# Performance work log

Measured on AMD Instinct MI355X. Metric: run time of the kernel, lower is better.

Reference implementation:

```python
import jax, jax.numpy as jnp
import numpy as np

B, T, C = 2, 2048, 1024
H, M = 16, 64
D = C // H  # head_dim = 64


def setup_inputs() -> dict:
    key = jax.random.key(0)
    ks = jax.random.split(key, 6)
    x = jax.random.normal(ks[0], (B, T, C), dtype=jnp.float32)
    Wqkv = jax.random.normal(ks[1], (3 * C, C), dtype=jnp.float32) / np.sqrt(C)
    bqkv = jax.random.normal(ks[2], (3 * C,), dtype=jnp.float32) * 0.02
    Wout = jax.random.normal(ks[3], (C, C), dtype=jnp.float32) / np.sqrt(C)
    bout = jax.random.normal(ks[4], (C,), dtype=jnp.float32) * 0.02
    proj = jax.random.normal(ks[5], (H, D, M), dtype=jnp.float32) / np.sqrt(D)
    return {"x": x, "Wqkv": Wqkv, "bqkv": bqkv, "Wout": Wout, "bout": bout, "proj": proj}


def reference(x, Wqkv, bqkv, Wout, bout, proj):
    b, t, c = x.shape
    h, d, m = proj.shape
    qkv = x @ Wqkv.T + bqkv                          # [B,T,3C]
    q, k, v = jnp.split(qkv, 3, axis=-1)
    # [B,T,C] -> [B,H,T,D]
    to_heads = lambda z: z.reshape(b, t, h, d).transpose(0, 2, 1, 3)
    q, k, v = to_heads(q), to_heads(k), to_heads(v)
    qf, kf, vf = q.astype(jnp.float32), k.astype(jnp.float32), v.astype(jnp.float32)
    pf = proj.astype(jnp.float32)
    q_prime = jax.nn.relu(jnp.einsum('bhtd,hdm->bhtm', qf, pf))
    k_prime = jax.nn.relu(jnp.einsum('bhtd,hdm->bhtm', kf, pf))
    k_cumsum = jnp.cumsum(k_prime, axis=2)                        # [B,H,T,M]
    kv_prod = jnp.einsum('bhtm,bhtd->bhtmd', k_prime, vf)          # [B,H,T,M,D]
    kv_cumsum = jnp.cumsum(kv_prod, axis=2)                        # [B,H,T,M,D]
    context = jnp.einsum('bhtm,bhtmd->bhtd', q_prime, kv_cumsum)   # [B,H,T,D]
    norm = jnp.einsum('bhtm,bhtm->bht', q_prime, k_cumsum)         # [B,H,T]
    out = context / (norm[..., None] + 1e-6)
    out = out.astype(x.dtype).transpose(0, 2, 1, 3).reshape(b, t, c)
    return out @ Wout.T + bout
```

## Files before the change

### kernel.cpp

```cpp
#include <hip/hip_runtime.h>
#include <cstddef>

#define B_  2
#define T_  2048
#define C_  1024
#define H_  16
#define D_  64
#define M_  64
#define NC_ 32
#define CH_ 64

typedef __attribute__((ext_vector_type(8))) short bf16x8;
typedef __attribute__((ext_vector_type(4))) float f32x4;

__device__ __forceinline__ ushort f2bf(float f) {
    union { float f; unsigned u; } v; v.f = f;
    unsigned r = v.u + 0x7FFF + ((v.u >> 16) & 1);
    return (ushort)(r >> 16);
}
__device__ __forceinline__ float bf2f(ushort u) {
    union { unsigned u; float f; } x; x.u = ((unsigned)u) << 16; return x.f;
}

__device__ __forceinline__ void gld_lds16(const ushort* g, ushort* lds) {
    __builtin_amdgcn_global_load_lds(
        (const __attribute__((address_space(1))) unsigned int*)g,
        (__attribute__((address_space(3))) unsigned int*)lds,
        16, 0, 0);
}

__device__ __forceinline__ bf16x8 frag_ld(const ushort* lds, int row16, int k0, int lane) {
    int r = row16 + (lane & 15);
    int byte = ((k0 * 2) + ((lane >> 4) << 4)) ^ ((r & 7) << 4);
    return *(const bf16x8*)((const char*)lds + r * 128 + byte);
}

#define VMCNT(n) asm volatile("s_waitcnt vmcnt(" #n ")" ::: "memory")
#define BAR() do { __builtin_amdgcn_s_barrier(); __builtin_amdgcn_sched_barrier(0); } while (0)

#define SEG1_ 256
#define SEG2_ 512
#define SEG3_ 1536
#define SEG4_ 1792
#define NPREP_ 1804

__global__ __launch_bounds__(256) void prep_all(
    const float* __restrict__ x, const float* __restrict__ Wqkv,
    const float* __restrict__ bqkv, const float* __restrict__ Wout,
    const float* __restrict__ proj,
    ushort* __restrict__ Wbt, ushort* __restrict__ xbf,
    ushort* __restrict__ WoutBf, float* __restrict__ bbig)
{
    __shared__ float Ws[64 * 128];
    __shared__ float Ps[64 * 64];
    const int blk = blockIdx.x, t = threadIdx.x;
    if (blk < SEG1_) {
        const int sel = blk >> 7, h = (blk >> 3) & 15, cc = blk & 7;
        const int rowbase = sel * 1024 + h * 64;
        {
            const int r0 = t >> 5, cq = t & 31;
#pragma unroll
            for (int k = 0; k < 8; ++k) {
                int r = r0 + 8 * k;
                *(float4*)&Ws[r * 128 + cq * 4] =
                    *(const float4*)&Wqkv[(size_t)(rowbase + r) * 1024 + cc * 128 + cq * 4];
            }
        }
#pragma unroll
        for (int k = 0; k < 4; ++k) {
            int i4 = t + 256 * k;
            *(float4*)&Ps[i4 * 4] = *(const float4*)&proj[h * 4096 + i4 * 4];
        }
        __syncthreads();
#pragma unroll
        for (int k = 0; k < 2; ++k) {
            int id = t + 256 * k;
            int m4 = id >> 5, c4 = id & 31;
            float4 a0 = {0.f,0.f,0.f,0.f}, a1 = a0, a2 = a0, a3 = a0;
            for (int d = 0; d < 64; ++d) {
                float4 w = *(const float4*)&Ws[d * 128 + c4 * 4];
                float4 p = *(const float4*)&Ps[d * 64 + m4 * 4];
                a0.x += p.x*w.x; a0.y += p.x*w.y; a0.z += p.x*w.z; a0.w += p.x*w.w;
                a1.x += p.y*w.x; a1.y += p.y*w.y; a1.z += p.y*w.z; a1.w += p.y*w.w;
                a2.x += p.z*w.x; a2.y += p.z*w.y; a2.z += p.z*w.z; a2.w += p.z*w.w;
                a3.x += p.w*w.x; a3.y += p.w*w.y; a3.z += p.w*w.z; a3.w += p.w*w.w;
            }
            size_t obase = (size_t)(rowbase + m4 * 4) * 1024 + cc * 128 + c4 * 4;
            ushort4 o0 = { f2bf(a0.x), f2bf(a0.y), f2bf(a0.z), f2bf(a0.w) };
            ushort4 o1 = { f2bf(a1.x), f2bf(a1.y), f2bf(a1.z), f2bf(a1.w) };
            ushort4 o2 = { f2bf(a2.x), f2bf(a2.y), f2bf(a2.z), f2bf(a2.w) };
            ushort4 o3 = { f2bf(a3.x), f2bf(a3.y), f2bf(a3.z), f2bf(a3.w) };
            *(ushort4*)&Wbt[obase]          = o0;
            *(ushort4*)&Wbt[obase + 1024]   = o1;
            *(ushort4*)&Wbt[obase + 2048]   = o2;
            *(ushort4*)&Wbt[obase + 3072]   = o3;
        }
    } else if (blk < SEG2_) {
        int bo = blk - SEG1_;
#pragma unroll
        for (int pass = 0; pass < 4; ++pass) {
            int i4 = bo * 1024 + pass * 256 + t;
            float4 v = ((const float4*)Wqkv)[524288 + i4];
            ushort4 o = { f2bf(v.x), f2bf(v.y), f2bf(v.z), f2bf(v.w) };
            ((ushort4*)(Wbt + 2097152))[i4] = o;
        }
    } else if (blk < SEG3_) {
        int bo = blk - SEG2_;
#pragma unroll
        for (int pass = 0; pass < 4; ++pass) {
            int i4 = bo * 1024 + pass * 256 + t;
            float4 v = ((const float4*)x)[i4];
            ushort4 o = { f2bf(v.x), f2bf(v.y), f2bf(v.z), f2bf(v.w) };
            ((ushort4*)xbf)[i4] = o;
        }
    } else if (blk < SEG4_) {
        int bo = blk - SEG3_;
#pragma unroll
        for (int pass = 0; pass < 4; ++pass) {
            int i4 = bo * 1024 + pass * 256 + t;
            float4 v = ((const float4*)Wout)[i4];
            ushort4 o = { f2bf(v.x), f2bf(v.y), f2bf(v.z), f2bf(v.w) };
            ((ushort4*)WoutBf)[i4] = o;
        }
    } else {
        int j = (blk - SEG4_) * 256 + t;
        if (j < 2048) {
            int sel = j >> 10, hm = j & 1023, h = hm >> 6, m = hm & 63;
            const float* b = bqkv + sel * C_ + h * D_;
            const float* p = proj + (size_t)h * D_ * M_ + m;
            float acc = 0.f;
#pragma unroll 8
            for (int d = 0; d < D_; ++d) acc += b[d] * p[(size_t)d * M_];
            bbig[j] = acc;
        } else {
            bbig[j] = bqkv[j];
        }
    }
}

__device__ __forceinline__ void stage_G0(const ushort* __restrict__ Ag, const ushort* __restrict__ Bg,
                                         ushort* Abuf, ushort* Bbuf,
                                         int m0, int n0, int K, int kcol, int w, int lane) {
    const int l8 = lane >> 3, lc = (lane & 7) * 8;
#pragma unroll
    for (int i = 0; i < 4; ++i) {
        int c = w * 4 + i;
        if (c < 8) {
            int fr = (c < 4) ? c * 8 : 64 + (c - 4) * 8;
            int r = fr + l8;
            int cs = lc ^ ((r & 7) << 3);
            gld_lds16(Ag + (size_t)(m0 + r) * K + kcol + cs, Abuf + fr * 64);
        } else {
            int cb = c - 8, g = cb / 6, k8 = cb - g * 6;
            int fr = g * 96 + k8 * 8;
            int r = fr + l8;
            int cs = lc ^ ((r & 7) << 3);
            gld_lds16(Bg + (size_t)(n0 + r) * K + kcol + cs, Bbuf + fr * 64);
        }
    }
}

__device__ __forceinline__ void stage_G1(const ushort* __restrict__ Ag, const ushort* __restrict__ Bg,
                                         ushort* Abuf, ushort* Bbuf,
                                         int m0, int n0, int K, int kcol, int w, int lane) {
    const int l8 = lane >> 3, lc = (lane & 7) * 8;
#pragma unroll
    for (int i = 0; i < 3; ++i) {
        int cb = w * 3 + i, g = cb / 6, k8 = cb - g * 6;
        int fr = g * 96 + 48 + k8 * 8;
        int r = fr + l8;
        int cs = lc ^ ((r & 7) << 3);
        gld_lds16(Bg + (size_t)(n0 + r) * K + kcol + cs, Bbuf + fr * 64);
    }
    {
        int fr = (w < 4) ? 32 + w * 8 : 96 + (w - 4) * 8;
        int r = fr + l8;
        int cs = lc ^ ((r & 7) << 3);
        gld_lds16(Ag + (size_t)(m0 + r) * K + kcol + cs, Abuf + fr * 64);
    }
}

__device__ __forceinline__ void phase_mfma(const ushort* Abuf, const ushort* Bbuf,
                                           f32x4 (&acc)[4][6], int wr, int wc, int lane,
                                           int Mh, int Nh) {
    bf16x8 a[2][2], b[3][2];
#pragma unroll
    for (int i = 0; i < 2; ++i)
#pragma unroll
        for (int ks = 0; ks < 2; ++ks)
            a[i][ks] = frag_ld(Abuf, wr + Mh * 32 + i * 16, ks * 32, lane);
#pragma unroll
    for (int j = 0; j < 3; ++j)
#pragma unroll
        for (int ks = 0; ks < 2; ++ks)
            b[j][ks] = frag_ld(Bbuf, wc + Nh * 48 + j * 16, ks * 32, lane);
    __builtin_amdgcn_s_setprio(1);
#pragma unroll
    for (int ks = 0; ks < 2; ++ks)
#pragma unroll
        for (int i = 0; i < 2; ++i)
#pragma unroll
            for (int j = 0; j < 3; ++j)
                acc[Mh * 2 + i][Nh * 3 + j] = __builtin_amdgcn_mfma_f32_16x16x32_bf16(
                    a[i][ks], b[j][ks], acc[Mh * 2 + i][Nh * 3 + j], 0, 0, 0);
    __builtin_amdgcn_s_setprio(0);
}

__global__ __launch_bounds__(512) void gemm_8phase(
    const ushort* __restrict__ A, const ushort* __restrict__ Bt,
    const float* __restrict__ bias, ushort* __restrict__ Cout,
    int M, int N, int K, int reluLimit)
{
    __shared__ __align__(16) ushort lds[65536];

    const int tid = threadIdx.x, w = tid >> 6, lane = tid & 63;
    const int m0 = blockIdx.y * 128, n0 = blockIdx.x * 384;
    const int wr = (w >> 2) * 64, wc = (w & 3) * 96;
    f32x4 acc[4][6] = {};
    const int NT = K / 64;

    stage_G0(A, Bt, lds, lds + 16384, m0, n0, K, 0, w, lane);
    stage_G1(A, Bt, lds, lds + 16384, m0, n0, K, 0, w, lane);

    for (int kt = 0; kt < NT - 1; ++kt) {
        const int p = kt & 1;
        ushort* Acur = lds + p * 8192;
        ushort* Anxt = lds + (p ^ 1) * 8192;
        ushort* Bcur = lds + 16384 + p * 24576;
        ushort* Bnxt = lds + 16384 + (p ^ 1) * 24576;
        const int kc1 = (kt + 1) * 64;
        VMCNT(4); BAR();
        stage_G0(A, Bt, Anxt, Bnxt, m0, n0, K, kc1, w, lane);
        phase_mfma(Acur, Bcur, acc, wr, wc, lane, 0, 0);
        VMCNT(5); BAR();
        phase_mfma(Acur, Bcur, acc, wr, wc, lane, 0, 1);
        VMCNT(4); BAR();
        stage_G1(A, Bt, Anxt, Bnxt, m0, n0, K, kc1, w, lane);
        phase_mfma(Acur, Bcur, acc, wr, wc, lane, 1, 0);
        phase_mfma(Acur, Bcur, acc, wr, wc, lane, 1, 1);
    }
    {
        const int p = (NT - 1) & 1;
        ushort* Acur = lds + p * 8192;
        ushort* Bcur = lds + 16384 + p * 24576;
        VMCNT(4); BAR();
        phase_mfma(Acur, Bcur, acc, wr, wc, lane, 0, 0);
        VMCNT(1); BAR();
        phase_mfma(Acur, Bcur, acc, wr, wc, lane, 0, 1);
        VMCNT(0); BAR();
        phase_mfma(Acur, Bcur, acc, wr, wc, lane, 1, 0);
        phase_mfma(Acur, Bcur, acc, wr, wc, lane, 1, 1);
    }

    const int crow = (lane >> 4) * 4, ccol = lane & 15;
#pragma unroll
    for (int nj = 0; nj < 6; ++nj) {
        int col = n0 + wc + nj * 16 + ccol;
        float bv = bias[col];
        bool rl = col < reluLimit;
#pragma unroll
        for (int mi = 0; mi < 4; ++mi) {
#pragma unroll
            for (int rr = 0; rr < 4; ++rr) {
                int row = m0 + wr + mi * 16 + crow + rr;
                float v = acc[mi][nj][rr] + bv;
                if (rl) v = fmaxf(v, 0.f);
                Cout[(size_t)row * N + col] = f2bf(v);
            }
        }
    }
}

__device__ __forceinline__ void g2_stage_G0(const ushort* __restrict__ Ag, const ushort* __restrict__ Bg,
                                            ushort* Abuf, ushort* Bbuf,
                                            int m0, int n0, int K, int kcol, int w, int lane) {
    const int l8 = lane >> 3, lc = (lane & 7) * 8;
    {
        int rbase = (w < 4) ? w * 8 : 64 + (w - 4) * 8;
        int r = rbase + l8;
        int cs = lc ^ ((r & 7) << 3);
        gld_lds16(Ag + (size_t)(m0 + r) * K + kcol + cs, Abuf + rbase * 64);
    }
    {
        int rbase = (w >> 1) * 32 + (w & 1) * 8;
        int r = rbase + l8;
        int cs = lc ^ ((r & 7) << 3);
        gld_lds16(Bg + (size_t)(n0 + r) * K + kcol + cs, Bbuf + rbase * 64);
    }
}

__device__ __forceinline__ void g2_stage_G1(const ushort* __restrict__ Ag, const ushort* __restrict__ Bg,
                                            ushort* Abuf, ushort* Bbuf,
                                            int m0, int n0, int K, int kcol, int w, int lane) {
    const int l8 = lane >> 3, lc = (lane & 7) * 8;
    {
        int rbase = 16 + (w >> 1) * 32 + (w & 1) * 8;
        int r = rbase + l8;
        int cs = lc ^ ((r & 7) << 3);
        gld_lds16(Bg + (size_t)(n0 + r) * K + kcol + cs, Bbuf + rbase * 64);
    }
    {
        int rbase = (w < 4) ? 32 + w * 8 : 96 + (w - 4) * 8;
        int r = rbase + l8;
        int cs = lc ^ ((r & 7) << 3);
        gld_lds16(Ag + (size_t)(m0 + r) * K + kcol + cs, Abuf + rbase * 64);
    }
}

__device__ __forceinline__ void g2_phase(const ushort* Abuf, const ushort* Bbuf,
                                         f32x4 (&acc)[4][2], int wr, int wc, int lane,
                                         int Mh, int Nh) {
    bf16x8 a[2][2], b[2];
#pragma unroll
    for (int i = 0; i < 2; ++i)
#pragma unroll
        for (int ks = 0; ks < 2; ++ks)
            a[i][ks] = frag_ld(Abuf, wr + Mh * 32 + i * 16, ks * 32, lane);
#pragma unroll
    for (int ks = 0; ks < 2; ++ks)
        b[ks] = frag_ld(Bbuf, wc + Nh * 16, ks * 32, lane);
    __builtin_amdgcn_s_setprio(1);
#pragma unroll
    for (int ks = 0; ks < 2; ++ks)
#pragma unroll
        for (int i = 0; i < 2; ++i)
            acc[Mh * 2 + i][Nh] = __builtin_amdgcn_mfma_f32_16x16x32_bf16(
                a[i][ks], b[ks], acc[Mh * 2 + i][Nh], 0, 0, 0);
    __builtin_amdgcn_s_setprio(0);
}

__global__ __launch_bounds__(512, 4) void gemm2_8phase(
    const ushort* __restrict__ A, const ushort* __restrict__ Bt,
    const float* __restrict__ bias, float* __restrict__ Cout,
    int M, int N, int K)
{
    __shared__ __align__(16) ushort lds[32768];

    const int tid = threadIdx.x, w = tid >> 6, lane = tid & 63;
    const int m0 = blockIdx.y * 128, n0 = blockIdx.x * 128;
    const int wr = (w >> 2) * 64, wc = (w & 3) * 32;
    f32x4 acc[4][2] = {};
    const int NT = K / 64;

    g2_stage_G0(A, Bt, lds, lds + 16384, m0, n0, K, 0, w, lane);
    g2_stage_G1(A, Bt, lds, lds + 16384, m0, n0, K, 0, w, lane);

    for (int kt = 0; kt < NT - 1; ++kt) {
        const int p = kt & 1;
        ushort* Acur = lds + p * 8192;
        ushort* Anxt = lds + (p ^ 1) * 8192;
        ushort* Bcur = lds + 16384 + p * 8192;
        ushort* Bnxt = lds + 16384 + (p ^ 1) * 8192;
        const int kc1 = (kt + 1) * 64;
        VMCNT(2); BAR();
        g2_stage_G0(A, Bt, Anxt, Bnxt, m0, n0, K, kc1, w, lane);
        g2_phase(Acur, Bcur, acc, wr, wc, lane, 0, 0);
        VMCNT(3); BAR();
        g2_phase(Acur, Bcur, acc, wr, wc, lane, 0, 1);
        VMCNT(2); BAR();
        g2_stage_G1(A, Bt, Anxt, Bnxt, m0, n0, K, kc1, w, lane);
        g2_phase(Acur, Bcur, acc, wr, wc, lane, 1, 0);
        g2_phase(Acur, Bcur, acc, wr, wc, lane, 1, 1);
    }
    {
        const int p = (NT - 1) & 1;
        ushort* Acur = lds + p * 8192;
        ushort* Bcur = lds + 16384 + p * 8192;
        VMCNT(2); BAR();
        g2_phase(Acur, Bcur, acc, wr, wc, lane, 0, 0);
        VMCNT(1); BAR();
        g2_phase(Acur, Bcur, acc, wr, wc, lane, 0, 1);
        VMCNT(0); BAR();
        g2_phase(Acur, Bcur, acc, wr, wc, lane, 1, 0);
        g2_phase(Acur, Bcur, acc, wr, wc, lane, 1, 1);
    }

    const int crow = (lane >> 4) * 4, ccol = lane & 15;
#pragma unroll
    for (int nj = 0; nj < 2; ++nj) {
        int col = n0 + wc + nj * 16 + ccol;
        float bv = bias[col];
#pragma unroll
        for (int mi = 0; mi < 4; ++mi) {
#pragma unroll
            for (int rr = 0; rr < 4; ++rr) {
                int row = m0 + wr + mi * 16 + crow + rr;
                Cout[(size_t)row * N + col] = acc[mi][nj][rr] + bv;
            }
        }
    }
}

__global__ __launch_bounds__(256) void chunk_kv_mfma(
    const ushort* __restrict__ out1, ushort* __restrict__ VtG,
    ushort* __restrict__ StB, float* __restrict__ sks)
{
    __shared__ unsigned Tl[64 * 76];
    __shared__ ushort Ktb[64 * 64];
    __shared__ ushort Vtb[64 * 64];
    __shared__ float skp[4][64];
    const int blk = blockIdx.x, c = blk & 31, bh = blk >> 5;
    const int b = bh >> 4, h = bh & 15, t0 = c * CH_;
    const int tid = threadIdx.x, wave = tid >> 6, lane = tid & 63;
    const ushort* kg = out1 + (size_t)(b * T_ + t0) * 3072 + C_ + h * D_;
    const ushort* vg = kg + C_;

#pragma unroll
    for (int it = 0; it < 2; ++it) {
        int i = tid + it * 256, r = i >> 3, sl = i & 7;
        bf16x8 v = *(const bf16x8*)(kg + (size_t)r * 3072 + sl * 8);
        unsigned* dst = &Tl[r * 76 + sl * 8];
        uint4 w0 = { (ushort)v[0], (ushort)v[1], (ushort)v[2], (ushort)v[3] };
        uint4 w1 = { (ushort)v[4], (ushort)v[5], (ushort)v[6], (ushort)v[7] };
        *(uint4*)dst = w0;
        *(uint4*)(dst + 4) = w1;
    }
    __syncthreads();
    {
        int m = tid >> 2, tc = tid & 3;
        bf16x8 va, vb;
        float s = 0.f;
#pragma unroll
        for (int k = 0; k < 8; ++k) {
            ushort u = (ushort)Tl[(tc * 16 + k) * 76 + m];
            va[k] = (short)u; s += bf2f(u);
        }
#pragma unroll
        for (int k = 0; k < 8; ++k) {
            ushort u = (ushort)Tl[(tc * 16 + 8 + k) * 76 + m];
            vb[k] = (short)u; s += bf2f(u);
        }
        skp[tc][m] = s;
        int b0 = (tc * 32) ^ ((m & 7) << 4);
        int b1 = (tc * 32 + 16) ^ ((m & 7) << 4);
        *(bf16x8*)((char*)Ktb + m * 128 + b0) = va;
        *(bf16x8*)((char*)Ktb + m * 128 + b1) = vb;
    }
    __syncthreads();
#pragma unroll
    for (int it = 0; it < 2; ++it) {
        int i = tid + it * 256, r = i >> 3, sl = i & 7;
        bf16x8 v = *(const bf16x8*)(vg + (size_t)r * 3072 + sl * 8);
        unsigned* dst = &Tl[r * 76 + sl * 8];
        uint4 w0 = { (ushort)v[0], (ushort)v[1], (ushort)v[2], (ushort)v[3] };
        uint4 w1 = { (ushort)v[4], (ushort)v[5], (ushort)v[6], (ushort)v[7] };
        *(uint4*)dst = w0;
        *(uint4*)(dst + 4) = w1;
    }
    __syncthreads();
    {
        int d = tid >> 2, tc = tid & 3;
        bf16x8 va, vb;
#pragma unroll
        for (int k = 0; k < 8; ++k) va[k] = (short)(ushort)Tl[(tc * 16 + k) * 76 + d];
#pragma unroll
        for (int k = 0; k < 8; ++k) vb[k] = (short)(ushort)Tl[(tc * 16 + 8 + k) * 76 + d];
        int b0 = (tc * 32) ^ ((d & 7) << 4);
        int b1 = (tc * 32 + 16) ^ ((d & 7) << 4);
        *(bf16x8*)((char*)Vtb + d * 128 + b0) = va;
        *(bf16x8*)((char*)Vtb + d * 128 + b1) = vb;
        ushort* og = VtG + (size_t)blk * 4096 + d * 64 + tc * 16;
        *(bf16x8*)og = va;
        *(bf16x8*)(og + 8) = vb;
    }
    __syncthreads();
    const int wr = wave * 16, g = lane >> 4, ccol = lane & 15;
    f32x4 acc[4] = {};
#pragma unroll
    for (int k0 = 0; k0 < 64; k0 += 32) {
        bf16x8 av = frag_ld(Vtb, wr, k0, lane);
#pragma unroll
        for (int j = 0; j < 4; ++j)
            acc[j] = __builtin_amdgcn_mfma_f32_16x16x32_bf16(av, frag_ld(Ktb, j * 16, k0, lane), acc[j], 0, 0, 0);
    }
    ushort* stg = StB + (size_t)blk * 4096;
#pragma unroll
    for (int j = 0; j < 4; ++j)
#pragma unroll
        for (int r = 0; r < 4; ++r)
            stg[(wr + g * 4 + r) * 64 + j * 16 + ccol] = f2bf(acc[j][r]);
    if (tid < 64)
        sks[(size_t)blk * 64 + tid] = skp[0][tid] + skp[1][tid] + skp[2][tid] + skp[3][tid];
}

__global__ __launch_bounds__(256) void chunk_scan2(const ushort* __restrict__ StB,
                                                   const float* __restrict__ sks,
                                                   ushort* __restrict__ Sbf,
                                                   ushort* __restrict__ skb) {
    if (blockIdx.x < 512) {
        int id = blockIdx.x * 256 + threadIdx.x;
        int bh = id >> 12, e = id & 4095;
        const ushort* p = StB + (size_t)bh * NC_ * 4096 + e;
        ushort* q = Sbf + (size_t)bh * NC_ * 4096 + e;
        float run = 0.f;
        for (int c = 0; c < NC_; ++c) {
            q[(size_t)c * 4096] = f2bf(run);
            run += bf2f(p[(size_t)c * 4096]);
        }
    } else {
        int id2 = (blockIdx.x - 512) * 256 + threadIdx.x;
        int bh = id2 >> 6, m = id2 & 63;
        const float* p = sks + (size_t)bh * NC_ * 64 + m;
        ushort* q = skb + (size_t)bh * NC_ * 64 + m;
        float run = 0.f;
        for (int c = 0; c < NC_; ++c) {
            q[c * 64] = f2bf(run);
            run += p[c * 64];
        }
    }
}

__global__ __launch_bounds__(256) void chunk_attn_mfma(
    const ushort* __restrict__ out1, const ushort* __restrict__ VtG,
    const ushort* __restrict__ Sbf, const ushort* __restrict__ skb,
    ushort* __restrict__ attnBf)
{
    __shared__ ushort Ql[64 * 64];
    __shared__ ushort Kl[64 * 64];
    __shared__ ushort Vl[64 * 64];
    __shared__ ushort Al[64 * 64];
    __shared__ ushort Sl[80 * 64];
    const int blk = blockIdx.x, c = blk & 31, bh = blk >> 5;
    const int b = bh >> 4, h = bh & 15, t0 = c * CH_;
    const int tid = threadIdx.x, wave = tid >> 6, lane = tid & 63;
    const ushort* qg  = out1 + (size_t)(b * T_ + t0) * 3072 + h * D_;
    const ushort* kg  = qg + C_;
    const ushort* vtg = VtG + (size_t)blk * 4096;
    const ushort* sbg = Sbf + (size_t)blk * 4096;
#pragma unroll
    for (int it = 0; it < 2; ++it) {
        int i = tid + it * 256, r = i >> 3, sl = i & 7;
        int lo = (sl * 16) ^ ((r & 7) << 4);
        *(bf16x8*)((char*)Ql + r * 128 + lo) = *(const bf16x8*)(qg + (size_t)r * 3072 + sl * 8);
        *(bf16x8*)((char*)Kl + r * 128 + lo) = *(const bf16x8*)(kg + (size_t)r * 3072 + sl * 8);
        *(bf16x8*)((char*)Vl + r * 128 + lo) = *(const bf16x8*)(vtg + r * 64 + sl * 8);
        *(bf16x8*)((char*)Sl + r * 128 + lo) = *(const bf16x8*)(sbg + r * 64 + sl * 8);
    }
    if (tid < 8)
        *(bf16x8*)((char*)Sl + 64 * 128 + tid * 16) = *(const bf16x8*)(skb + (size_t)blk * 64 + tid * 8);
    __syncthreads();

    const int wr = wave * 16, g = lane >> 4, ccol = lane & 15;
    f32x4 accA[4] = {};
#pragma unroll
    for (int k0 = 0; k0 < 64; k0 += 32) {
        bf16x8 aq = frag_ld(Ql, wr, k0, lane);
#pragma unroll
        for (int j = 0; j < 4; ++j)
            accA[j] = __builtin_amdgcn_mfma_f32_16x16x32_bf16(aq, frag_ld(Kl, j * 16, k0, lane), accA[j], 0, 0, 0);
    }
    float rsum[4] = {0.f, 0.f, 0.f, 0.f};
#pragma unroll
    for (int j = 0; j < 4; ++j) {
#pragma unroll
        for (int r = 0; r < 4; ++r) {
            int tl = wr + g * 4 + r, sl2 = j * 16 + ccol;
            float v = (sl2 <= tl) ? accA[j][r] : 0.f;
            rsum[r] += v;
            *(ushort*)((char*)Al + tl * 128 + ((sl2 * 2) ^ ((tl & 7) << 4))) = f2bf(v);
        }
    }
#pragma unroll
    for (int r = 0; r < 4; ++r) {
        rsum[r] += __shfl_xor(rsum[r], 1);
        rsum[r] += __shfl_xor(rsum[r], 2);
        rsum[r] += __shfl_xor(rsum[r], 4);
        rsum[r] += __shfl_xor(rsum[r], 8);
    }
    f32x4 accC[4] = {};
    f32x4 accE = {};
#pragma unroll
    for (int k0 = 0; k0 < 64; k0 += 32) {
        bf16x8 aa = frag_ld(Al, wr, k0, lane);
#pragma unroll
        for (int j = 0; j < 4; ++j)
            accC[j] = __builtin_amdgcn_mfma_f32_16x16x32_bf16(aa, frag_ld(Vl, j * 16, k0, lane), accC[j], 0, 0, 0);
    }
#pragma unroll
    for (int k0 = 0; k0 < 64; k0 += 32) {
        bf16x8 aq = frag_ld(Ql, wr, k0, lane);
#pragma unroll
        for (int j = 0; j < 4; ++j)
            accC[j] = __builtin_amdgcn_mfma_f32_16x16x32_bf16(aq, frag_ld(Sl, j * 16, k0, lane), accC[j], 0, 0, 0);
        accE = __builtin_amdgcn_mfma_f32_16x16x32_bf16(aq, frag_ld(Sl, 64, k0, lane), accE, 0, 0, 0);
    }
    ushort* og = attnBf + (size_t)(b * T_ + t0) * C_ + h * D_;
#pragma unroll
    for (int r = 0; r < 4; ++r) {
        float nq = __shfl(accE[r], (lane & 48));
        float inv = 1.f / (nq + rsum[r] + 1e-6f);
        int tl = wr + g * 4 + r;
#pragma unroll
        for (int j = 0; j < 4; ++j)
            og[(size_t)tl * C_ + j * 16 + ccol] = f2bf(accC[j][r] * inv);
    }
}

extern "C" void kernel_launch(void* const* d_in, const int* in_sizes, int n_in,
                              void* d_out, int out_size, void* d_ws, size_t ws_size,
                              hipStream_t stream) {
    (void)in_sizes; (void)n_in; (void)out_size; (void)ws_size;
    const float* x    = (const float*)d_in[0];
    const float* Wqkv = (const float*)d_in[1];
    const float* bqkv = (const float*)d_in[2];
    const float* Wout = (const float*)d_in[3];
    const float* bout = (const float*)d_in[4];
    const float* proj = (const float*)d_in[5];
    float* out = (float*)d_out;
    char* ws = (char*)d_ws;

    ushort* Wbt    = (ushort*)(ws);
    ushort* xbf    = (ushort*)(ws + (6ull  << 20));
    ushort* WoutBf = (ushort*)(ws + (14ull << 20));
    ushort* attnBf = (ushort*)(ws + (16ull << 20));
    float*  bbig   = (float*) (ws + (24ull << 20));
    ushort* out1   = (ushort*)(ws + (25ull << 20));
    ushort* VtG    = (ushort*)(ws + (49ull << 20));
    ushort* StB    = (ushort*)(ws + (57ull << 20));
    ushort* Sbf    = (ushort*)(ws + (65ull << 20));
    float*  sks    = (float*) (ws + (73ull << 20));
    ushort* skb    = (ushort*)(ws + (74ull << 20));

    prep_all<<<NPREP_, 256, 0, stream>>>(x, Wqkv, bqkv, Wout, proj,
                                         Wbt, xbf, WoutBf, bbig);
    gemm_8phase<<<dim3(8, 32), 512, 0, stream>>>(xbf, Wbt, bbig, out1,
                                                 4096, 3072, 1024, 2048);
    chunk_kv_mfma<<<1024, 256, 0, stream>>>(out1, VtG, StB, sks);
    chunk_scan2<<<520, 256, 0, stream>>>(StB, sks, Sbf, skb);
    chunk_attn_mfma<<<1024, 256, 0, stream>>>(out1, VtG, Sbf, skb, attnBf);
    gemm2_8phase<<<dim3(8, 32), 512, 0, stream>>>(attnBf, WoutBf, bout, out,
                                                  4096, 1024, 1024);
}
```

Measured before the change: 88.79 us.

## Unify QKV and output GEMMs on smaller-tile template and reuse LDS fragments

New measurement: 86.76 us. 2.3% less time.

```diff
diff --git a/kernel.cpp b/kernel.cpp
--- a/kernel.cpp
+++ b/kernel.cpp
@@ -138,142 +138,9 @@
     }
 }
 
-__device__ __forceinline__ void stage_G0(const ushort* __restrict__ Ag, const ushort* __restrict__ Bg,
-                                         ushort* Abuf, ushort* Bbuf,
-                                         int m0, int n0, int K, int kcol, int w, int lane) {
-    const int l8 = lane >> 3, lc = (lane & 7) * 8;
-#pragma unroll
-    for (int i = 0; i < 4; ++i) {
-        int c = w * 4 + i;
-        if (c < 8) {
-            int fr = (c < 4) ? c * 8 : 64 + (c - 4) * 8;
-            int r = fr + l8;
-            int cs = lc ^ ((r & 7) << 3);
-            gld_lds16(Ag + (size_t)(m0 + r) * K + kcol + cs, Abuf + fr * 64);
-        } else {
-            int cb = c - 8, g = cb / 6, k8 = cb - g * 6;
-            int fr = g * 96 + k8 * 8;
-            int r = fr + l8;
-            int cs = lc ^ ((r & 7) << 3);
-            gld_lds16(Bg + (size_t)(n0 + r) * K + kcol + cs, Bbuf + fr * 64);
-        }
-    }
-}
-
-__device__ __forceinline__ void stage_G1(const ushort* __restrict__ Ag, const ushort* __restrict__ Bg,
-                                         ushort* Abuf, ushort* Bbuf,
-                                         int m0, int n0, int K, int kcol, int w, int lane) {
-    const int l8 = lane >> 3, lc = (lane & 7) * 8;
-#pragma unroll
-    for (int i = 0; i < 3; ++i) {
-        int cb = w * 3 + i, g = cb / 6, k8 = cb - g * 6;
-        int fr = g * 96 + 48 + k8 * 8;
-        int r = fr + l8;
-        int cs = lc ^ ((r & 7) << 3);
-        gld_lds16(Bg + (size_t)(n0 + r) * K + kcol + cs, Bbuf + fr * 64);
-    }
-    {
-        int fr = (w < 4) ? 32 + w * 8 : 96 + (w - 4) * 8;
-        int r = fr + l8;
-        int cs = lc ^ ((r & 7) << 3);
-        gld_lds16(Ag + (size_t)(m0 + r) * K + kcol + cs, Abuf + fr * 64);
-    }
-}
-
-__device__ __forceinline__ void phase_mfma(const ushort* Abuf, const ushort* Bbuf,
-                                           f32x4 (&acc)[4][6], int wr, int wc, int lane,
-                                           int Mh, int Nh) {
-    bf16x8 a[2][2], b[3][2];
-#pragma unroll
-    for (int i = 0; i < 2; ++i)
-#pragma unroll
-        for (int ks = 0; ks < 2; ++ks)
-            a[i][ks] = frag_ld(Abuf, wr + Mh * 32 + i * 16, ks * 32, lane);
-#pragma unroll
-    for (int j = 0; j < 3; ++j)
-#pragma unroll
-        for (int ks = 0; ks < 2; ++ks)
-            b[j][ks] = frag_ld(Bbuf, wc + Nh * 48 + j * 16, ks * 32, lane);
-    __builtin_amdgcn_s_setprio(1);
-#pragma unroll
-    for (int ks = 0; ks < 2; ++ks)
-#pragma unroll
-        for (int i = 0; i < 2; ++i)
-#pragma unroll
-            for (int j = 0; j < 3; ++j)
-                acc[Mh * 2 + i][Nh * 3 + j] = __builtin_amdgcn_mfma_f32_16x16x32_bf16(
-                    a[i][ks], b[j][ks], acc[Mh * 2 + i][Nh * 3 + j], 0, 0, 0);
-    __builtin_amdgcn_s_setprio(0);
-}
-
-__global__ __launch_bounds__(512) void gemm_8phase(
-    const ushort* __restrict__ A, const ushort* __restrict__ Bt,
-    const float* __restrict__ bias, ushort* __restrict__ Cout,
-    int M, int N, int K, int reluLimit)
-{
-    __shared__ __align__(16) ushort lds[65536];
-
-    const int tid = threadIdx.x, w = tid >> 6, lane = tid & 63;
-    const int m0 = blockIdx.y * 128, n0 = blockIdx.x * 384;
-    const int wr = (w >> 2) * 64, wc = (w & 3) * 96;
-    f32x4 acc[4][6] = {};
-    const int NT = K / 64;
-
-    stage_G0(A, Bt, lds, lds + 16384, m0, n0, K, 0, w, lane);
-    stage_G1(A, Bt, lds, lds + 16384, m0, n0, K, 0, w, lane);
-
-    for (int kt = 0; kt < NT - 1; ++kt) {
-        const int p = kt & 1;
-        ushort* Acur = lds + p * 8192;
-        ushort* Anxt = lds + (p ^ 1) * 8192;
-        ushort* Bcur = lds + 16384 + p * 24576;
-        ushort* Bnxt = lds + 16384 + (p ^ 1) * 24576;
-        const int kc1 = (kt + 1) * 64;
-        VMCNT(4); BAR();
-        stage_G0(A, Bt, Anxt, Bnxt, m0, n0, K, kc1, w, lane);
-        phase_mfma(Acur, Bcur, acc, wr, wc, lane, 0, 0);
-        VMCNT(5); BAR();
-        phase_mfma(Acur, Bcur, acc, wr, wc, lane, 0, 1);
-        VMCNT(4); BAR();
-        stage_G1(A, Bt, Anxt, Bnxt, m0, n0, K, kc1, w, lane);
-        phase_mfma(Acur, Bcur, acc, wr, wc, lane, 1, 0);
-        phase_mfma(Acur, Bcur, acc, wr, wc, lane, 1, 1);
-    }
-    {
-        const int p = (NT - 1) & 1;
-        ushort* Acur = lds + p * 8192;
-        ushort* Bcur = lds + 16384 + p * 24576;
-        VMCNT(4); BAR();
-        phase_mfma(Acur, Bcur, acc, wr, wc, lane, 0, 0);
-        VMCNT(1); BAR();
-        phase_mfma(Acur, Bcur, acc, wr, wc, lane, 0, 1);
-        VMCNT(0); BAR();
-        phase_mfma(Acur, Bcur, acc, wr, wc, lane, 1, 0);
-        phase_mfma(Acur, Bcur, acc, wr, wc, lane, 1, 1);
-    }
-
-    const int crow = (lane >> 4) * 4, ccol = lane & 15;
-#pragma unroll
-    for (int nj = 0; nj < 6; ++nj) {
-        int col = n0 + wc + nj * 16 + ccol;
-        float bv = bias[col];
-        bool rl = col < reluLimit;
-#pragma unroll
-        for (int mi = 0; mi < 4; ++mi) {
-#pragma unroll
-            for (int rr = 0; rr < 4; ++rr) {
-                int row = m0 + wr + mi * 16 + crow + rr;
-                float v = acc[mi][nj][rr] + bv;
-                if (rl) v = fmaxf(v, 0.f);
-                Cout[(size_t)row * N + col] = f2bf(v);
-            }
-        }
-    }
-}
-
-__device__ __forceinline__ void g2_stage_G0(const ushort* __restrict__ Ag, const ushort* __restrict__ Bg,
-                                            ushort* Abuf, ushort* Bbuf,
-                                            int m0, int n0, int K, int kcol, int w, int lane) {
+__device__ __forceinline__ void g_stage_G0(const ushort* __restrict__ Ag, const ushort* __restrict__ Bg,
+                                           ushort* Abuf, ushort* Bbuf,
+                                           int m0, int n0, int K, int kcol, int w, int lane) {
     const int l8 = lane >> 3, lc = (lane & 7) * 8;
     {
         int rbase = (w < 4) ? w * 8 : 64 + (w - 4) * 8;
@@ -289,9 +156,9 @@
     }
 }
 
-__device__ __forceinline__ void g2_stage_G1(const ushort* __restrict__ Ag, const ushort* __restrict__ Bg,
-                                            ushort* Abuf, ushort* Bbuf,
-                                            int m0, int n0, int K, int kcol, int w, int lane) {
+__device__ __forceinline__ void g_stage_G1(const ushort* __restrict__ Ag, const ushort* __restrict__ Bg,
+                                           ushort* Abuf, ushort* Bbuf,
+                                           int m0, int n0, int K, int kcol, int w, int lane) {
     const int l8 = lane >> 3, lc = (lane & 7) * 8;
     {
         int rbase = 16 + (w >> 1) * 32 + (w & 1) * 8;
@@ -307,18 +174,20 @@
     }
 }
 
-__device__ __forceinline__ void g2_phase(const ushort* Abuf, const ushort* Bbuf,
-                                         f32x4 (&acc)[4][2], int wr, int wc, int lane,
-                                         int Mh, int Nh) {
-    bf16x8 a[2][2], b[2];
+__device__ __forceinline__ void lda2(const ushort* Abuf, bf16x8 (&a)[2][2], int wr, int Mh, int lane) {
 #pragma unroll
     for (int i = 0; i < 2; ++i)
 #pragma unroll
         for (int ks = 0; ks < 2; ++ks)
             a[i][ks] = frag_ld(Abuf, wr + Mh * 32 + i * 16, ks * 32, lane);
+}
+__device__ __forceinline__ void g_ldb(const ushort* Bbuf, bf16x8 (&b)[2], int wc, int Nh, int lane) {
 #pragma unroll
     for (int ks = 0; ks < 2; ++ks)
         b[ks] = frag_ld(Bbuf, wc + Nh * 16, ks * 32, lane);
+}
+__device__ __forceinline__ void g_mfma(f32x4 (&acc)[4][2], const bf16x8 (&a)[2][2],
+                                       const bf16x8 (&b)[2], int Mh, int Nh) {
     __builtin_amdgcn_s_setprio(1);
 #pragma unroll
     for (int ks = 0; ks < 2; ++ks)
@@ -329,10 +198,11 @@
     __builtin_amdgcn_s_setprio(0);
 }
 
-__global__ __launch_bounds__(512, 4) void gemm2_8phase(
+template <bool BF16OUT>
+__global__ __launch_bounds__(512, 4) void gemm_u8p(
     const ushort* __restrict__ A, const ushort* __restrict__ Bt,
-    const float* __restrict__ bias, float* __restrict__ Cout,
-    int M, int N, int K)
+    const float* __restrict__ bias, void* __restrict__ Cout,
+    int M, int N, int K, int reluLimit)
 {
     __shared__ __align__(16) ushort lds[32768];
 
@@ -342,8 +212,8 @@
     f32x4 acc[4][2] = {};
     const int NT = K / 64;
 
-    g2_stage_G0(A, Bt, lds, lds + 16384, m0, n0, K, 0, w, lane);
-    g2_stage_G1(A, Bt, lds, lds + 16384, m0, n0, K, 0, w, lane);
+    g_stage_G0(A, Bt, lds, lds + 16384, m0, n0, K, 0, w, lane);
+    g_stage_G1(A, Bt, lds, lds + 16384, m0, n0, K, 0, w, lane);
 
     for (int kt = 0; kt < NT - 1; ++kt) {
         const int p = kt & 1;
@@ -352,27 +222,37 @@
         ushort* Bcur = lds + 16384 + p * 8192;
         ushort* Bnxt = lds + 16384 + (p ^ 1) * 8192;
         const int kc1 = (kt + 1) * 64;
+        bf16x8 a[2][2], a2[2][2], b[2], b2[2];
         VMCNT(2); BAR();
-        g2_stage_G0(A, Bt, Anxt, Bnxt, m0, n0, K, kc1, w, lane);
-        g2_phase(Acur, Bcur, acc, wr, wc, lane, 0, 0);
+        g_stage_G0(A, Bt, Anxt, Bnxt, m0, n0, K, kc1, w, lane);
+        lda2(Acur, a, wr, 0, lane);
+        g_ldb(Bcur, b, wc, 0, lane);
+        g_mfma(acc, a, b, 0, 0);
         VMCNT(3); BAR();
-        g2_phase(Acur, Bcur, acc, wr, wc, lane, 0, 1);
+        g_ldb(Bcur, b2, wc, 1, lane);
+        g_mfma(acc, a, b2, 0, 1);
         VMCNT(2); BAR();
-        g2_stage_G1(A, Bt, Anxt, Bnxt, m0, n0, K, kc1, w, lane);
-        g2_phase(Acur, Bcur, acc, wr, wc, lane, 1, 0);
-        g2_phase(Acur, Bcur, acc, wr, wc, lane, 1, 1);
+        g_stage_G1(A, Bt, Anxt, Bnxt, m0, n0, K, kc1, w, lane);
+        lda2(Acur, a2, wr, 1, lane);
+        g_mfma(acc, a2, b, 1, 0);
+        g_mfma(acc, a2, b2, 1, 1);
     }
     {
         const int p = (NT - 1) & 1;
         ushort* Acur = lds + p * 8192;
         ushort* Bcur = lds + 16384 + p * 8192;
+        bf16x8 a[2][2], a2[2][2], b[2], b2[2];
         VMCNT(2); BAR();
-        g2_phase(Acur, Bcur, acc, wr, wc, lane, 0, 0);
+        lda2(Acur, a, wr, 0, lane);
+        g_ldb(Bcur, b, wc, 0, lane);
+        g_mfma(acc, a, b, 0, 0);
         VMCNT(1); BAR();
-        g2_phase(Acur, Bcur, acc, wr, wc, lane, 0, 1);
+        g_ldb(Bcur, b2, wc, 1, lane);
+        g_mfma(acc, a, b2, 0, 1);
         VMCNT(0); BAR();
-        g2_phase(Acur, Bcur, acc, wr, wc, lane, 1, 0);
-        g2_phase(Acur, Bcur, acc, wr, wc, lane, 1, 1);
+        lda2(Acur, a2, wr, 1, lane);
+        g_mfma(acc, a2, b, 1, 0);
+        g_mfma(acc, a2, b2, 1, 1);
     }
 
     const int crow = (lane >> 4) * 4, ccol = lane & 15;
@@ -380,12 +260,18 @@
     for (int nj = 0; nj < 2; ++nj) {
         int col = n0 + wc + nj * 16 + ccol;
         float bv = bias[col];
+        bool rl = col < reluLimit;
 #pragma unroll
         for (int mi = 0; mi < 4; ++mi) {
 #pragma unroll
             for (int rr = 0; rr < 4; ++rr) {
                 int row = m0 + wr + mi * 16 + crow + rr;
-                Cout[(size_t)row * N + col] = acc[mi][nj][rr] + bv;
+                float v = acc[mi][nj][rr] + bv;
+                if (rl) v = fmaxf(v, 0.f);
+                if (BF16OUT)
+                    ((ushort*)Cout)[(size_t)row * N + col] = f2bf(v);
+                else
+                    ((float*)Cout)[(size_t)row * N + col] = v;
             }
         }
     }
@@ -623,11 +509,11 @@
 
     prep_all<<<NPREP_, 256, 0, stream>>>(x, Wqkv, bqkv, Wout, proj,
                                          Wbt, xbf, WoutBf, bbig);
-    gemm_8phase<<<dim3(8, 32), 512, 0, stream>>>(xbf, Wbt, bbig, out1,
-                                                 4096, 3072, 1024, 2048);
+    gemm_u8p<true><<<dim3(24, 32), 512, 0, stream>>>(xbf, Wbt, bbig, out1,
+                                                     4096, 3072, 1024, 2048);
     chunk_kv_mfma<<<1024, 256, 0, stream>>>(out1, VtG, StB, sks);
     chunk_scan2<<<520, 256, 0, stream>>>(StB, sks, Sbf, skb);
     chunk_attn_mfma<<<1024, 256, 0, stream>>>(out1, VtG, Sbf, skb, attnBf);
-    gemm2_8phase<<<dim3(8, 32), 512, 0, stream>>>(attnBf, WoutBf, bout, out,
-                                                  4096, 1024, 1024);
-}
+    gemm_u8p<false><<<dim3(8, 32), 512, 0, stream>>>(attnBf, WoutBf, bout, out,
+                                                     4096, 1024, 1024, 0);
+}
```
